# Optimization experiments

Measured on AMD Instinct MI355X. Metric: run time of the kernel, lower is better.

## Reference

```python
import jax, jax.numpy as jnp
import numpy as np

B = 256        # graphs
NODES = 116    # nodes per view per graph
FEAT = 115     # node feature dim
LENN = 6670    # edges per view per graph (116*115/2)
SEG2 = 13456   # raw edges per graph in input (2*LENN + 116 discarded)
HID = 128      # hidden_channels
HC = 512       # hc


def setup_inputs() -> dict:
    key = jax.random.key(0)
    ks = jax.random.split(key, 12)
    x = jax.random.normal(ks[0], (B * 2 * NODES, FEAT), jnp.float32)
    # per-graph edge layout: [6670 FC edges | 6670 SC edges | 116 dummy]
    off = (2 * NODES) * jnp.arange(B, dtype=jnp.int32)  # [B]
    fc = jax.random.randint(ks[1], (2, B, LENN), 0, NODES, dtype=jnp.int32) + off[None, :, None]
    sc = jax.random.randint(ks[2], (2, B, LENN), 0, NODES, dtype=jnp.int32) + off[None, :, None] + NODES
    dummy = jnp.zeros((2, B, SEG2 - 2 * LENN), jnp.int32) + off[None, :, None]
    edge_index = jnp.concatenate([fc, sc, dummy], axis=2).reshape(2, B * SEG2)
    edge_weight = jax.random.uniform(ks[3], (B * SEG2,), jnp.float32)
    batch = jnp.repeat(jnp.arange(B, dtype=jnp.int32), 2 * NODES)
    s = 1.0 / np.sqrt(FEAT)
    W1 = jax.random.uniform(ks[4], (FEAT, HID), jnp.float32, -s, s)
    b1 = jnp.zeros((HID,), jnp.float32)
    W2 = jax.random.uniform(ks[5], (FEAT, HID), jnp.float32, -s, s)
    b2 = jnp.zeros((HID,), jnp.float32)
    s6 = 1.0 / np.sqrt(2 * NODES)
    W6 = jax.random.uniform(ks[6], (2 * NODES, HC), jnp.float32, -s6, s6)
    b6 = jax.random.uniform(ks[7], (HC,), jnp.float32, -s6, s6)
    s7 = 1.0 / np.sqrt(HC)
    W7 = jax.random.uniform(ks[8], (HC, 1), jnp.float32, -s7, s7)
    b7 = jax.random.uniform(ks[9], (1,), jnp.float32, -s7, s7)
    return dict(x=x, edge_index=edge_index, edge_weight=edge_weight, batch=batch,
                W1=W1, b1=b1, W2=W2, b2=b2, W6=W6, b6=b6, W7=W7, b7=b7)


def _gcn_conv(x, ei, ew, W, b, num_nodes):
    """PyG GCNConv: D^-1/2 (A+I) D^-1/2 X W + b (self-loop weight 1)."""
    h = x @ W                                   # [N, HID]
    src, dst = ei[0], ei[1]
    deg = jax.ops.segment_sum(ew, dst, num_segments=num_nodes) + 1.0  # +1 self-loop
    dinv = jax.lax.rsqrt(deg)                   # [N]
    norm = dinv[src] * ew * dinv[dst]           # [E]
    out = jax.ops.segment_sum(h[src] * norm[:, None], dst, num_segments=num_nodes)
    out = out + (dinv * dinv)[:, None] * h      # self-loop message
    return out + b


def reference(x, edge_index, edge_weight, batch, W1, b1, W2, b2, W6, b6, W7, b7):
    gidx = jnp.arange(B, dtype=edge_index.dtype)
    ei = edge_index.reshape(2, B, SEG2)
    ew = edge_weight.reshape(B, SEG2)
    # de-offset per-graph edges into per-view node index spaces (116 nodes/graph)
    ei_fc = (ei[:, :, :LENN] - NODES * gidx[None, :, None]).reshape(2, B * LENN)
    ei_sc = (ei[:, :, LENN:2 * LENN] - NODES * (gidx + 1)[None, :, None]).reshape(2, B * LENN)
    ew_fc = ew[:, :LENN].reshape(-1)
    ew_sc = ew[:, LENN:2 * LENN].reshape(-1)
    xr = x.reshape(B, 2 * NODES, FEAT)
    node_fc = xr[:, :NODES].reshape(B * NODES, FEAT)
    node_sc = xr[:, NODES:].reshape(B * NODES, FEAT)
    N = B * NODES
    x1 = _gcn_conv(node_fc, ei_fc, ew_fc, W1, b1, N).max(axis=1)  # [B*116]
    x2 = _gcn_conv(node_sc, ei_sc, ew_sc, W2, b2, N).max(axis=1)  # [B*116]
    feat = jnp.stack([x1, x2], axis=1).reshape(B, 2 * NODES)      # flatten()
    # dropout p=0.5 is identity in eval mode
    h = jax.nn.relu(feat @ W6 + b6)
    return h @ W7 + b7  # [B, 1]
```

## Files before the change

### kernel.cpp

```cpp
#include <hip/hip_runtime.h>


#define NB 256
#define NODES 116
#define FEAT 115
#define LENN 6670
#define SEG2 13456
#define HID 128
#define HC 512
#define AF_STR 120

typedef float f32x4 __attribute__((ext_vector_type(4)));
typedef short short8 __attribute__((ext_vector_type(8)));
typedef __bf16 bf16x8 __attribute__((ext_vector_type(8)));

#define MFMA16(a, b, c) __builtin_amdgcn_mfma_f32_16x16x32_bf16( \
    __builtin_bit_cast(bf16x8, (a)), __builtin_bit_cast(bf16x8, (b)), (c), 0, 0, 0)

#define OFF_ALO 32768
#define OFF_BHI 65536
#define OFF_BLO 98304
#define OFF_PMAX 131072
#define OFF_DINV 133120
#define LDS_BYTES 133632

__device__ __forceinline__ unsigned short f2bf_s(float f) {
  return __builtin_bit_cast(unsigned short, (__bf16)f);
}
__device__ __forceinline__ float bf2f_s(unsigned short h) {
  return __builtin_bit_cast(float, (unsigned)h << 16);
}
__device__ __forceinline__ void cvt4(const float* v, uint2& hi, uint2& lo) {
  unsigned short h[4], l[4];
#pragma unroll
  for (int j = 0; j < 4; ++j) {
    h[j] = f2bf_s(v[j]);
    l[j] = f2bf_s(v[j] - bf2f_s(h[j]));
  }
  hi.x = (unsigned)h[0] | ((unsigned)h[1] << 16);
  hi.y = (unsigned)h[2] | ((unsigned)h[3] << 16);
  lo.x = (unsigned)l[0] | ((unsigned)l[1] << 16);
  lo.y = (unsigned)l[2] | ((unsigned)l[3] << 16);
}
__device__ __forceinline__ int kperm(int k) {
  return (k & ~31) | (k & 3) | (((k >> 2) & 3) << 3) | (((k >> 4) & 1) << 2);
}
__device__ __forceinline__ int kb64(int t) {
  return ((t & 3) << 4) | (((t >> 2) & 1) << 3) | ((t >> 3) << 6);
}
__device__ __forceinline__ int swzb(int row, int kbyte) {
  return row * 256 + (kbyte ^ ((row & 7) << 4));
}
__device__ __forceinline__ f32x4 splat4(float f) {
  f32x4 r = {f, f, f, f};
  return r;
}

__global__ __launch_bounds__(1024, 1) void k_fused(
    const float* __restrict__ x, const int* __restrict__ ei,
    const float* __restrict__ ew,
    const float* __restrict__ W1, const float* __restrict__ b1,
    const float* __restrict__ W2, const float* __restrict__ b2,
    float* __restrict__ featws)
{
  __shared__ __align__(16) char sm[LDS_BYTES];
  float* Afp   = (float*)(sm + OFF_BHI);
  float* dinv  = (float*)(sm + OFF_DINV);
  float* pmaxp = (float*)(sm + OFF_PMAX);
  const int bid = blockIdx.x;
  const int g = bid >> 1, v = bid & 1;
  const int tid = threadIdx.x;

  {
    f32x4 z = splat4(0.f);
    f32x4* p = (f32x4*)(sm + OFF_BHI);
    for (int i = tid; i < 3480; i += 1024) p[i] = z;
  }
  __syncthreads();

  const int eoff = g * SEG2 + v * LENN;
  const int nbase = g * 232 + v * 116;

  {
    const int* __restrict__ srcp = ei + eoff;
    const int* __restrict__ dstp = ei + (size_t)NB * SEG2 + eoff;
    const float* __restrict__ wp = ew + eoff;
    for (int q = tid; q < (LENN / 2); q += 1024) {
      int2 s2 = ((const int2*)srcp)[q];
      int2 d2 = ((const int2*)dstp)[q];
      float2 w2 = ((const float2*)wp)[q];
      atomicAdd(&Afp[(d2.x - nbase) * AF_STR + (s2.x - nbase)], w2.x);
      atomicAdd(&Afp[(d2.y - nbase) * AF_STR + (s2.y - nbase)], w2.y);
    }
  }
  __syncthreads();

  if (tid < 4 * NODES) {
    const int r = tid >> 2, q = tid & 3;
    const float* row = Afp + r * AF_STR + q * 29;
    float s = 0.f;
#pragma unroll
    for (int j = 0; j < 29; ++j) s += row[j];
    s += __shfl_xor(s, 1, 64);
    s += __shfl_xor(s, 2, 64);
    if (q == 0) dinv[r] = rsqrtf(s + 1.0f);
  }
  __syncthreads();

  float xr[4][4];
  {
    const float* __restrict__ xg = x + (size_t)nbase * FEAT;
#pragma unroll
    for (int i = 0; i < 4; ++i) {
      int u = tid + (i << 10);
      int t = u >> 7, c = u & 127;
#pragma unroll
      for (int j = 0; j < 4; ++j) {
        int s = 4 * t + j;
        xr[i][j] = (c < FEAT && s < NODES) ? xg[s * FEAT + c] : 0.f;
      }
    }
  }

  for (int p = tid; p < NODES * 32; p += 1024) {
    const int row = p >> 5;
    const int t = p & 31;
    float tv[4] = {0.f, 0.f, 0.f, 0.f};
    if (t < 29) {
      const float dr = dinv[row];
      f32x4 q4 = *(const f32x4*)(Afp + row * AF_STR + (t << 2));
#pragma unroll
      for (int j = 0; j < 4; ++j) {
        const int cc = (t << 2) + j;
        float q = q4[j] * (dr * dinv[cc]);
        if (cc == row) q += dr * dr;
        tv[j] = q;
      }
    }
    uint2 hi, lo;
    cvt4(tv, hi, lo);
    const int byte = swzb(row, kb64(t));
    *(uint2*)(sm + byte) = hi;
    *(uint2*)(sm + OFF_ALO + byte) = lo;
  }
  __syncthreads();

#pragma unroll
  for (int i = 0; i < 4; ++i) {
    int u = tid + (i << 10);
    int t = u >> 7, c = u & 127;
    uint2 hi, lo;
    cvt4(xr[i], hi, lo);
    int byte = swzb(c, kb64(t));
    *(uint2*)(sm + OFF_BHI + byte) = hi;
    *(uint2*)(sm + OFF_BLO + byte) = lo;
  }
  __syncthreads();

  const int lane = tid & 63, w = tid >> 6;
  const int mg = w >> 2, ng = w & 3;
  const int rA0 = (mg << 5) + (lane & 15), rA1 = rA0 + 16;
  const int rB0 = (ng << 5) + (lane & 15), rB1 = rB0 + 16;
  const int kb = (lane >> 4) << 4;

  float wr[4][4];
  {
    const float* __restrict__ Wv = v ? W2 : W1;
#pragma unroll
    for (int i = 0; i < 4; ++i) {
      int u = tid + (i << 10);
      int t = u >> 7, c = u & 127;
#pragma unroll
      for (int j = 0; j < 4; ++j) {
        int k = 4 * t + j;
        wr[i][j] = (k < FEAT) ? Wv[(size_t)k * HID + c] : 0.f;
      }
    }
  }

  f32x4 acc00 = splat4(0.f), acc01 = splat4(0.f);
  f32x4 acc10 = splat4(0.f), acc11 = splat4(0.f);

#pragma unroll
  for (int kc = 0; kc < 4; ++kc) {
    const int ko = (kc << 6) + kb;
    short8 a0h = *(const short8*)(sm + swzb(rA0, ko));
    short8 a0l = *(const short8*)(sm + OFF_ALO + swzb(rA0, ko));
    short8 a1h = *(const short8*)(sm + swzb(rA1, ko));
    short8 a1l = *(const short8*)(sm + OFF_ALO + swzb(rA1, ko));
    short8 b0h = *(const short8*)(sm + OFF_BHI + swzb(rB0, ko));
    short8 b0l = *(const short8*)(sm + OFF_BLO + swzb(rB0, ko));
    short8 b1h = *(const short8*)(sm + OFF_BHI + swzb(rB1, ko));
    short8 b1l = *(const short8*)(sm + OFF_BLO + swzb(rB1, ko));
    acc00 = MFMA16(a0h, b0h, acc00); acc00 = MFMA16(a0l, b0h, acc00); acc00 = MFMA16(a0h, b0l, acc00);
    acc01 = MFMA16(a0h, b1h, acc01); acc01 = MFMA16(a0l, b1h, acc01); acc01 = MFMA16(a0h, b1l, acc01);
    acc10 = MFMA16(a1h, b0h, acc10); acc10 = MFMA16(a1l, b0h, acc10); acc10 = MFMA16(a1h, b0l, acc10);
    acc11 = MFMA16(a1h, b1h, acc11); acc11 = MFMA16(a1l, b1h, acc11); acc11 = MFMA16(a1h, b1l, acc11);
  }
  __syncthreads();

  {
#pragma unroll
    for (int mt = 0; mt < 2; ++mt)
#pragma unroll
      for (int nt = 0; nt < 2; ++nt)
#pragma unroll
        for (int r2 = 0; r2 < 4; ++r2) {
          f32x4 a = (mt == 0) ? (nt == 0 ? acc00 : acc01)
                              : (nt == 0 ? acc10 : acc11);
          float f = a[r2];
          int row = (mg << 5) + (mt << 4) + ((lane >> 4) << 2) + r2;
          int col = (ng << 5) + (nt << 4) + (lane & 15);
          unsigned short hi = f2bf_s(f);
          unsigned short lo = f2bf_s(f - bf2f_s(hi));
          int byte = swzb(row, kperm(col) << 1);
          *(unsigned short*)(sm + byte) = hi;
          *(unsigned short*)(sm + OFF_ALO + byte) = lo;
        }
#pragma unroll
    for (int i = 0; i < 4; ++i) {
      int u = tid + (i << 10);
      int t = u >> 7, c = u & 127;
      uint2 hi, lo;
      cvt4(wr[i], hi, lo);
      int byte = swzb(c, kb64(t));
      *(uint2*)(sm + OFF_BHI + byte) = hi;
      *(uint2*)(sm + OFF_BLO + byte) = lo;
    }
  }
  __syncthreads();

  {
    const float* __restrict__ bv = v ? b2 : b1;
    float bb0 = bv[(ng << 5) + (lane & 15)];
    float bb1 = bv[(ng << 5) + 16 + (lane & 15)];
    acc00 = splat4(bb0); acc01 = splat4(bb1);
    acc10 = splat4(bb0); acc11 = splat4(bb1);
  }
#pragma unroll
  for (int kc = 0; kc < 4; ++kc) {
    const int ko = (kc << 6) + kb;
    short8 a0h = *(const short8*)(sm + swzb(rA0, ko));
    short8 a0l = *(const short8*)(sm + OFF_ALO + swzb(rA0, ko));
    short8 a1h = *(const short8*)(sm + swzb(rA1, ko));
    short8 a1l = *(const short8*)(sm + OFF_ALO + swzb(rA1, ko));
    short8 b0h = *(const short8*)(sm + OFF_BHI + swzb(rB0, ko));
    short8 b0l = *(const short8*)(sm + OFF_BLO + swzb(rB0, ko));
    short8 b1h = *(const short8*)(sm + OFF_BHI + swzb(rB1, ko));
    short8 b1l = *(const short8*)(sm + OFF_BLO + swzb(rB1, ko));
    acc00 = MFMA16(a0h, b0h, acc00); acc00 = MFMA16(a0l, b0h, acc00); acc00 = MFMA16(a0h, b0l, acc00);
    acc01 = MFMA16(a0h, b1h, acc01); acc01 = MFMA16(a0l, b1h, acc01); acc01 = MFMA16(a0h, b1l, acc01);
    acc10 = MFMA16(a1h, b0h, acc10); acc10 = MFMA16(a1l, b0h, acc10); acc10 = MFMA16(a1h, b0l, acc10);
    acc11 = MFMA16(a1h, b1h, acc11); acc11 = MFMA16(a1l, b1h, acc11); acc11 = MFMA16(a1h, b1l, acc11);
  }

#pragma unroll
  for (int mt = 0; mt < 2; ++mt)
#pragma unroll
    for (int r2 = 0; r2 < 4; ++r2) {
      f32x4 aN0 = (mt == 0) ? acc00 : acc10;
      f32x4 aN1 = (mt == 0) ? acc01 : acc11;
      float m = fmaxf(aN0[r2], aN1[r2]);
      m = fmaxf(m, __shfl_xor(m, 1, 64));
      m = fmaxf(m, __shfl_xor(m, 2, 64));
      m = fmaxf(m, __shfl_xor(m, 4, 64));
      m = fmaxf(m, __shfl_xor(m, 8, 64));
      if ((lane & 15) == 0) {
        int row = (mg << 5) + (mt << 4) + ((lane >> 4) << 2) + r2;
        pmaxp[(ng << 7) + row] = m;
      }
    }
  __syncthreads();
  if (tid < NODES) {
    float m = fmaxf(fmaxf(pmaxp[tid], pmaxp[128 + tid]),
                    fmaxf(pmaxp[256 + tid], pmaxp[384 + tid]));
    featws[g * 232 + 2 * tid + v] = m;
  }
}

__global__ __launch_bounds__(1024) void k_mlp(
    const float* __restrict__ featws, const float* __restrict__ W6,
    const float* __restrict__ b6, const float* __restrict__ W7,
    const float* __restrict__ b7, float* __restrict__ out)
{
  __shared__ float sf[232];
  __shared__ float ph[512];
  __shared__ float red[8];
  const int g = blockIdx.x, tid = threadIdx.x;
  if (tid < 232) sf[tid] = featws[g * 232 + tid];
  __syncthreads();

  const int col = tid & 511, half = tid >> 9;
  const float* __restrict__ w6p = W6 + (size_t)(half * 116) * HC + col;
  const float* __restrict__ sfh = sf + half * 116;
  float p = 0.f;
#pragma unroll 4
  for (int k = 0; k < 116; ++k)
    p = fmaf(sfh[k], w6p[(size_t)k * HC], p);
  if (half) ph[col] = p;
  __syncthreads();

  if (!half) {
    float a = b6[col] + p + ph[col];
    a = fmaxf(a, 0.f) * W7[col];
#pragma unroll
    for (int off = 32; off >= 1; off >>= 1) a += __shfl_xor(a, off, 64);
    if ((tid & 63) == 0) red[tid >> 6] = a;
  }
  __syncthreads();
  if (tid == 0) {
    float t = b7[0];
#pragma unroll
    for (int i = 0; i < 8; ++i) t += red[i];
    out[g] = t;
  }
}

extern "C" void kernel_launch(void* const* d_in, const int* in_sizes, int n_in,
                              void* d_out, int out_size, void* d_ws, size_t ws_size,
                              hipStream_t stream)
{
  const float* x  = (const float*)d_in[0];
  const int*   ei = (const int*)d_in[1];
  const float* ew = (const float*)d_in[2];
  const float* W1 = (const float*)d_in[4];
  const float* b1 = (const float*)d_in[5];
  const float* W2 = (const float*)d_in[6];
  const float* b2 = (const float*)d_in[7];
  const float* W6 = (const float*)d_in[8];
  const float* b6 = (const float*)d_in[9];
  const float* W7 = (const float*)d_in[10];
  const float* b7 = (const float*)d_in[11];

  float* featws = (float*)d_ws;
  float* out    = (float*)d_out;

  hipLaunchKernelGGL(k_fused, dim3(2 * NB), dim3(1024), 0, stream,
                     x, ei, ew, W1, b1, W2, b2, featws);
  hipLaunchKernelGGL(k_mlp,   dim3(NB),     dim3(1024), 0, stream,
                     featws, W6, b6, W7, b7, out);
}
```

Before: 154.6 us.

## Hoist global loads earlier in fused GCN kernel and process two graphs per MLP block

```diff
diff --git a/kernel.cpp b/kernel.cpp
--- a/kernel.cpp
+++ b/kernel.cpp
@@ -76,10 +76,25 @@
     f32x4* p = (f32x4*)(sm + OFF_BHI);
     for (int i = tid; i < 3480; i += 1024) p[i] = z;
   }
-  __syncthreads();
 
   const int eoff = g * SEG2 + v * LENN;
   const int nbase = g * 232 + v * 116;
+
+  float xr[4][4];
+  {
+    const float* __restrict__ xg = x + (size_t)nbase * FEAT;
+#pragma unroll
+    for (int i = 0; i < 4; ++i) {
+      int u = tid + (i << 10);
+      int t = u >> 7, c = u & 127;
+#pragma unroll
+      for (int j = 0; j < 4; ++j) {
+        int s = 4 * t + j;
+        xr[i][j] = (c < FEAT && s < NODES) ? xg[s * FEAT + c] : 0.f;
+      }
+    }
+  }
+  __syncthreads();
 
   {
     const int* __restrict__ srcp = ei + eoff;
@@ -107,17 +122,17 @@
   }
   __syncthreads();
 
-  float xr[4][4];
-  {
-    const float* __restrict__ xg = x + (size_t)nbase * FEAT;
+  float wr[4][4];
+  {
+    const float* __restrict__ Wv = v ? W2 : W1;
 #pragma unroll
     for (int i = 0; i < 4; ++i) {
       int u = tid + (i << 10);
       int t = u >> 7, c = u & 127;
 #pragma unroll
       for (int j = 0; j < 4; ++j) {
-        int s = 4 * t + j;
-        xr[i][j] = (c < FEAT && s < NODES) ? xg[s * FEAT + c] : 0.f;
+        int k = 4 * t + j;
+        wr[i][j] = (k < FEAT) ? Wv[(size_t)k * HID + c] : 0.f;
       }
     }
   }
@@ -162,21 +177,6 @@
   const int rA0 = (mg << 5) + (lane & 15), rA1 = rA0 + 16;
   const int rB0 = (ng << 5) + (lane & 15), rB1 = rB0 + 16;
   const int kb = (lane >> 4) << 4;
-
-  float wr[4][4];
-  {
-    const float* __restrict__ Wv = v ? W2 : W1;
-#pragma unroll
-    for (int i = 0; i < 4; ++i) {
-      int u = tid + (i << 10);
-      int t = u >> 7, c = u & 127;
-#pragma unroll
-      for (int j = 0; j < 4; ++j) {
-        int k = 4 * t + j;
-        wr[i][j] = (k < FEAT) ? Wv[(size_t)k * HID + c] : 0.f;
-      }
-    }
-  }
 
   f32x4 acc00 = splat4(0.f), acc01 = splat4(0.f);
   f32x4 acc10 = splat4(0.f), acc11 = splat4(0.f);
@@ -283,36 +283,48 @@
     const float* __restrict__ b6, const float* __restrict__ W7,
     const float* __restrict__ b7, float* __restrict__ out)
 {
-  __shared__ float sf[232];
-  __shared__ float ph[512];
-  __shared__ float red[8];
-  const int g = blockIdx.x, tid = threadIdx.x;
-  if (tid < 232) sf[tid] = featws[g * 232 + tid];
+  __shared__ float sf[2][232];
+  __shared__ float ph[2][512];
+  __shared__ float red[2][8];
+  const int g0 = blockIdx.x << 1;
+  const int tid = threadIdx.x;
+  if (tid < 464) {
+    int gg = tid / 232, idx = tid - gg * 232;
+    sf[gg][idx] = featws[(g0 + gg) * 232 + idx];
+  }
   __syncthreads();
 
   const int col = tid & 511, half = tid >> 9;
   const float* __restrict__ w6p = W6 + (size_t)(half * 116) * HC + col;
-  const float* __restrict__ sfh = sf + half * 116;
-  float p = 0.f;
+  const float* __restrict__ s0 = sf[0] + half * 116;
+  const float* __restrict__ s1 = sf[1] + half * 116;
+  float p0 = 0.f, p1 = 0.f;
 #pragma unroll 4
-  for (int k = 0; k < 116; ++k)
-    p = fmaf(sfh[k], w6p[(size_t)k * HC], p);
-  if (half) ph[col] = p;
+  for (int k = 0; k < 116; ++k) {
+    float wv = w6p[(size_t)k * HC];
+    p0 = fmaf(s0[k], wv, p0);
+    p1 = fmaf(s1[k], wv, p1);
+  }
+  if (half) { ph[0][col] = p0; ph[1][col] = p1; }
   __syncthreads();
 
   if (!half) {
-    float a = b6[col] + p + ph[col];
-    a = fmaxf(a, 0.f) * W7[col];
-#pragma unroll
-    for (int off = 32; off >= 1; off >>= 1) a += __shfl_xor(a, off, 64);
-    if ((tid & 63) == 0) red[tid >> 6] = a;
-  }
-  __syncthreads();
-  if (tid == 0) {
+    float w7 = W7[col], bb = b6[col];
+    float a0 = fmaxf(bb + p0 + ph[0][col], 0.f) * w7;
+    float a1 = fmaxf(bb + p1 + ph[1][col], 0.f) * w7;
+#pragma unroll
+    for (int off = 32; off >= 1; off >>= 1) {
+      a0 += __shfl_xor(a0, off, 64);
+      a1 += __shfl_xor(a1, off, 64);
+    }
+    if ((tid & 63) == 0) { red[0][tid >> 6] = a0; red[1][tid >> 6] = a1; }
+  }
+  __syncthreads();
+  if (tid < 2) {
     float t = b7[0];
 #pragma unroll
-    for (int i = 0; i < 8; ++i) t += red[i];
-    out[g] = t;
+    for (int i = 0; i < 8; ++i) t += red[tid][i];
+    out[g0 + tid] = t;
   }
 }
 
@@ -337,6 +349,6 @@
 
   hipLaunchKernelGGL(k_fused, dim3(2 * NB), dim3(1024), 0, stream,
                      x, ei, ew, W1, b1, W2, b2, featws);
-  hipLaunchKernelGGL(k_mlp,   dim3(NB),     dim3(1024), 0, stream,
+  hipLaunchKernelGGL(k_mlp,   dim3(NB / 2), dim3(1024), 0, stream,
                      featws, W6, b6, W7, b7, out);
 }
```

After: 158.2 us. 1.02x slower.
